# Kernel optimization log

Measured on AMD Instinct MI355X. Metric: run time of the kernel, lower is better.

Reference implementation:

```python
import jax, jax.numpy as jnp
import numpy as np

NUM_LAYERS = 3
CHANNELS = 8
IN_CHANNELS = 8
MASK_OUT_STRIDE = 4


def resize_align_corners(x, oh, ow):
    # Bilinear resize with align_corners=True, x: [N, C, H, W]
    n, c, h, w = x.shape
    ys = jnp.linspace(0.0, h - 1.0, oh)
    xs = jnp.linspace(0.0, w - 1.0, ow)
    y0 = jnp.clip(jnp.floor(ys).astype(jnp.int32), 0, h - 2)
    x0 = jnp.clip(jnp.floor(xs).astype(jnp.int32), 0, w - 2)
    wy = (ys - y0.astype(ys.dtype)).astype(x.dtype)[None, None, :, None]
    wx = (xs - x0.astype(xs.dtype)).astype(x.dtype)[None, None, None, :]
    top = x[:, :, y0, :]
    bot = x[:, :, y0 + 1, :]
    row = top * (1.0 - wy) + bot * wy          # [n,c,oh,w]
    left = row[:, :, :, x0]
    right = row[:, :, :, x0 + 1]
    return left * (1.0 - wx) + right * wx       # [n,c,oh,ow]


def aligned_bilinear(t, factor):
    # Faithful port of adet.utils.comm.aligned_bilinear
    if factor == 1:
        return t
    h, w = t.shape[2], t.shape[3]
    t = jnp.pad(t, ((0, 0), (0, 0), (0, 1), (0, 1)), mode="edge")
    oh, ow = factor * h + 1, factor * w + 1
    t = resize_align_corners(t, oh, ow)
    p = factor // 2
    t = jnp.pad(t, ((0, 0), (0, 0), (p, 0), (p, 0)), mode="edge")
    return t[:, :, : oh - 1, : ow - 1]


def reference(mask_feats, mask_head_params, locations_inst, soi, im_inds, fpn_levels, mask_feat_stride):
    N, C, H, W = mask_feats.shape
    n_inst = mask_head_params.shape[0]
    # compute_locations at mask_feat_stride (x fastest, matching torch meshgrid order)
    half = mask_feat_stride // 2
    sx = jnp.arange(W, dtype=mask_feats.dtype) * mask_feat_stride + half
    sy = jnp.arange(H, dtype=mask_feats.dtype) * mask_feat_stride + half
    gy, gx = jnp.meshgrid(sy, sx, indexing="ij")
    locs = jnp.stack([gx.reshape(-1), gy.reshape(-1)], axis=1)  # [HW, 2]
    # relative coords, normalized by size-of-interest of instance's FPN level
    rel = locations_inst[:, None, :] - locs[None, :, :]          # [n, HW, 2]
    rel = jnp.transpose(rel, (0, 2, 1))                          # [n, 2, HW]
    rel = rel / soi[fpn_levels][:, None, None]
    feats = mask_feats[im_inds].reshape(n_inst, IN_CHANNELS, H * W)
    x = jnp.concatenate([rel.astype(mask_feats.dtype), feats], axis=1)  # [n, 10, HW]
    # parse_dynamic_params: split flat params into per-instance weights/biases
    wn = [(IN_CHANNELS + 2) * CHANNELS, CHANNELS * CHANNELS, CHANNELS * 1]
    bn = [CHANNELS, CHANNELS, 1]
    offs = np.cumsum([0] + wn + bn)
    parts = [mask_head_params[:, offs[i]:offs[i + 1]] for i in range(6)]
    w0 = parts[0].reshape(n_inst, CHANNELS, IN_CHANNELS + 2)
    w1 = parts[1].reshape(n_inst, CHANNELS, CHANNELS)
    w2 = parts[2].reshape(n_inst, 1, CHANNELS)
    b0, b1, b2 = parts[3], parts[4], parts[5]
    # per-instance dynamic MLP (1x1 grouped conv == batched matmul)
    x = jax.nn.relu(jnp.einsum("noi,nip->nop", w0, x) + b0[:, :, None])
    x = jax.nn.relu(jnp.einsum("noi,nip->nop", w1, x) + b1[:, :, None])
    x = jnp.einsum("noi,nip->nop", w2, x) + b2[:, :, None]
    logits = x.reshape(n_inst, 1, H, W)
    factor = int(mask_feat_stride // MASK_OUT_STRIDE)
    return aligned_bilinear(logits, factor)


def setup_inputs() -> dict:
    key = jax.random.key(0)
    k0, k1, k2, k3, k4 = jax.random.split(key, 5)
    N, C, H, W = 4, IN_CHANNELS, 128, 192
    n_inst = 128
    stride = 8
    num_gen_params = (IN_CHANNELS + 2) * CHANNELS + CHANNELS * CHANNELS + CHANNELS + CHANNELS + CHANNELS + 1  # 169
    mask_feats = jax.random.normal(k0, (N, C, H, W), dtype=jnp.float32)
    mask_head_params = jax.random.normal(k1, (n_inst, num_gen_params), dtype=jnp.float32) * 0.1
    locations_inst = jax.random.uniform(k2, (n_inst, 2), dtype=jnp.float32) * jnp.array([W * stride, H * stride], jnp.float32)
    soi = jnp.array([64.0, 128.0, 256.0, 512.0, 1024.0], jnp.float32)
    im_inds = jax.random.randint(k3, (n_inst,), 0, N)
    fpn_levels = jax.random.randint(k4, (n_inst,), 0, 5)
    return {
        "mask_feats": mask_feats,
        "mask_head_params": mask_head_params,
        "locations_inst": locations_inst,
        "soi": soi,
        "im_inds": im_inds,
        "fpn_levels": fpn_levels,
        "mask_feat_stride": stride,
    }
```

## Files before the change

### kernel.cpp

```cpp
#include <hip/hip_runtime.h>

#define HH 128
#define WW 192
#define HW (HH * WW)

typedef float f32x4 __attribute__((ext_vector_type(4)));

__device__ __forceinline__ float relu(float v) { return fmaxf(v, 0.0f); }


__global__ __launch_bounds__(256) void dmh_kernel(
    const float* __restrict__ mask_feats,
    const float* __restrict__ params,
    const float* __restrict__ locs,
    const float* __restrict__ soi,
    const int*   __restrict__ im_inds,
    const int*   __restrict__ fpn_levels,
    const int*   __restrict__ stride_p,
    float*       __restrict__ out)
{
    const int tid = threadIdx.x;
    const int c0 = blockIdx.x * 64;
    const int r0 = blockIdx.y * 32;
    const int n  = blockIdx.z;

    __shared__ float sW[176];
    __shared__ float tile[33 * 66];

    if (tid < 169) {
        float v = params[(size_t)n * 169 + tid];
        int d;
        if (tid < 80)       { int o = tid / 10, r = tid - o * 10;
                              d = (r == 0) ? o : (r == 1) ? (8 + o) : (24 + (r - 2) * 8 + o); }
        else if (tid < 144) { int t = tid - 80, o = t >> 3, i = t & 7; d = 88 + i * 8 + o; }
        else if (tid < 152) d = 152 + (tid - 144);
        else if (tid < 160) d = 16 + (tid - 152);
        else if (tid < 168) d = 160 + (tid - 160);
        else                d = 168;
        sW[d] = v;
    }

    const int   stride = *stride_p;
    const float half   = 0.5f * (float)stride;
    const float locx = locs[2 * n + 0];
    const float locy = locs[2 * n + 1];
    const float inv  = 1.0f / soi[fpn_levels[n]];
    const float* fb  = mask_feats + (size_t)im_inds[n] * 8 * HW;

    const int ir  = (tid >> 4) * 2;
    const int ic  = (tid & 15) * 4;
    const int rA  = r0 + ir;
    const int cc0 = c0 + ic;
    const float* fpA = fb + rA * WW + cc0;

    f32x4 xA[8], xB[8];
    #pragma unroll
    for (int ch = 0; ch < 8; ++ch) {
        xA[ch] = *reinterpret_cast<const f32x4*>(fpA + ch * HW);
        xB[ch] = *reinterpret_cast<const f32x4*>(fpA + ch * HW + WW);
    }

    __syncthreads();

    const f32x4* __restrict__ sW4 = reinterpret_cast<const f32x4*>(sW);

    {
        const float rxd = -(float)stride * inv;
        float rx[4];
        rx[0] = (locx - (float)(cc0 * stride) - half) * inv;
        rx[1] = rx[0] + rxd; rx[2] = rx[1] + rxd; rx[3] = rx[2] + rxd;
        const float ryA = (locy - (float)(rA * stride) - half) * inv;
        const float ryB = ryA - (float)stride * inv;

        f32x4 w0xL = sW4[0], w0xH = sW4[1];
        f32x4 w0yL = sW4[2], w0yH = sW4[3];
        f32x4 b0L  = sW4[4], b0H  = sW4[5];

        float hA[8][4], hB[8][4];
        #pragma unroll
        for (int o = 0; o < 8; ++o) {
            float wx = (o < 4) ? w0xL[o] : w0xH[o - 4];
            float wy = (o < 4) ? w0yL[o] : w0yH[o - 4];
            float b  = (o < 4) ? b0L[o]  : b0H[o - 4];
            float tA = fmaf(wy, ryA, b);
            float tB = fmaf(wy, ryB, b);
            #pragma unroll
            for (int j = 0; j < 4; ++j) {
                hA[o][j] = fmaf(wx, rx[j], tA);
                hB[o][j] = fmaf(wx, rx[j], tB);
            }
        }
        #pragma unroll
        for (int ch = 0; ch < 8; ++ch) {
            f32x4 wL = sW4[6 + 2 * ch];
            f32x4 wH = sW4[7 + 2 * ch];
            #pragma unroll
            for (int o = 0; o < 8; ++o) {
                float w = (o < 4) ? wL[o] : wH[o - 4];
                #pragma unroll
                for (int j = 0; j < 4; ++j) {
                    hA[o][j] = fmaf(w, xA[ch][j], hA[o][j]);
                    hB[o][j] = fmaf(w, xB[ch][j], hB[o][j]);
                }
            }
        }

        float aA[8][4], aB[8][4];
        {
            f32x4 b1L = sW4[40], b1H = sW4[41];
            #pragma unroll
            for (int o = 0; o < 8; ++o) {
                float b = (o < 4) ? b1L[o] : b1H[o - 4];
                #pragma unroll
                for (int j = 0; j < 4; ++j) { aA[o][j] = b; aB[o][j] = b; }
            }
        }
        #pragma unroll
        for (int i = 0; i < 8; ++i) {
            f32x4 wL = sW4[22 + 2 * i];
            f32x4 wH = sW4[23 + 2 * i];
            float vA[4], vB[4];
            #pragma unroll
            for (int j = 0; j < 4; ++j) { vA[j] = relu(hA[i][j]); vB[j] = relu(hB[i][j]); }
            #pragma unroll
            for (int o = 0; o < 8; ++o) {
                float w = (o < 4) ? wL[o] : wH[o - 4];
                #pragma unroll
                for (int j = 0; j < 4; ++j) {
                    aA[o][j] = fmaf(w, vA[j], aA[o][j]);
                    aB[o][j] = fmaf(w, vB[j], aB[o][j]);
                }
            }
        }

        f32x4 w2L = sW4[38], w2H = sW4[39];
        const float b2v = sW[168];
        float lgA[4] = {b2v, b2v, b2v, b2v};
        float lgB[4] = {b2v, b2v, b2v, b2v};
        #pragma unroll
        for (int o = 0; o < 8; ++o) {
            float w2 = (o < 4) ? w2L[o] : w2H[o - 4];
            #pragma unroll
            for (int j = 0; j < 4; ++j) {
                lgA[j] = fmaf(w2, relu(aA[o][j]), lgA[j]);
                lgB[j] = fmaf(w2, relu(aB[o][j]), lgB[j]);
            }
        }
        #pragma unroll
        for (int j = 0; j < 4; ++j) {
            tile[(ir + 1) * 66 + ic + 1 + j] = lgA[j];
            tile[(ir + 2) * 66 + ic + 1 + j] = lgB[j];
        }
    }

    if (tid < 97) {
        int r, c;
        if (tid < 65) { r = -1; c = tid - 1; }
        else          { r = tid - 65; c = -1; }
        int hr = min(max(r0 + r, 0), HH - 1);
        int hc = min(max(c0 + c, 0), WW - 1);
        const float* hfp = fb + hr * WW + hc;
        float rx  = (locx - (float)(hc * stride) - half) * inv;
        float ry2 = (locy - (float)(hr * stride) - half) * inv;
        float hh[8];
        #pragma unroll
        for (int o = 0; o < 8; ++o)
            hh[o] = fmaf(sW[o], rx, fmaf(sW[8 + o], ry2, sW[16 + o]));
        #pragma unroll
        for (int ch = 0; ch < 8; ++ch) {
            float x = hfp[ch * HW];
            #pragma unroll
            for (int o = 0; o < 8; ++o) hh[o] = fmaf(sW[24 + ch * 8 + o], x, hh[o]);
        }
        float aa[8];
        #pragma unroll
        for (int o = 0; o < 8; ++o) aa[o] = sW[160 + o];
        #pragma unroll
        for (int i = 0; i < 8; ++i) {
            float v = relu(hh[i]);
            #pragma unroll
            for (int o = 0; o < 8; ++o) aa[o] = fmaf(sW[88 + i * 8 + o], v, aa[o]);
        }
        float lg = sW[168];
        #pragma unroll
        for (int o = 0; o < 8; ++o) lg = fmaf(sW[152 + o], relu(aa[o]), lg);
        tile[(r + 1) * 66 + (c + 1)] = lg;
    }
    __syncthreads();

    const int kx = tid & 31;
    const int ky = tid >> 5;
    float* ob = out + ((size_t)n * 256 + 2 * r0) * 384 + 2 * c0 + 4 * kx;
    #pragma unroll
    for (int yy = 0; yy < 8; ++yy) {
        int yt = ky * 8 + yy;
        int iy = yt - 1;
        int rbl = iy >> 1;
        int fy = iy & 1;
        float wy0 = fy ? 0.5f : 1.0f;
        float wy1 = fy ? 0.5f : 0.0f;
        int sr  = rbl + 1;
        int sr2 = sr + fy;
        const float* ra = &tile[sr  * 66 + 2 * kx];
        const float* rc = &tile[sr2 * 66 + 2 * kx];
        float t0 = fmaf(wy1, rc[0], wy0 * ra[0]);
        float t1 = fmaf(wy1, rc[1], wy0 * ra[1]);
        float t2 = fmaf(wy1, rc[2], wy0 * ra[2]);
        f32x4 o4;
        o4.x = 0.5f * (t0 + t1);
        o4.y = t1;
        o4.z = 0.5f * (t1 + t2);
        o4.w = t2;
        __builtin_nontemporal_store(o4, reinterpret_cast<f32x4*>(ob + (size_t)yt * 384));
    }
}

extern "C" void kernel_launch(void* const* d_in, const int* in_sizes, int n_in,
                              void* d_out, int out_size, void* d_ws, size_t ws_size,
                              hipStream_t stream) {
    const float* mask_feats = (const float*)d_in[0];
    const float* params     = (const float*)d_in[1];
    const float* locs       = (const float*)d_in[2];
    const float* soi        = (const float*)d_in[3];
    const int*   im_inds    = (const int*)d_in[4];
    const int*   fpn_levels = (const int*)d_in[5];
    const int*   stride_p   = (const int*)d_in[6];
    float* out = (float*)d_out;

    dim3 grid(WW / 64, HH / 32, 128);
    dim3 block(256);
    dmh_kernel<<<grid, block, 0, stream>>>(
        mask_feats, params, locs, soi, im_inds, fpn_levels, stride_p, out);
}
```

Measured before the change: 21.28 us.

## Retile to full-width 16-row strips and drop scalar halo recomputation

Each block now covers a 16-row by full-width (192 column) strip instead of a 32x64 tile, so halo handling needs only one extra row above. That row is clamped, and the left column edge is handled by clamping the index in the upsampling stage. The scalar halo path run by 97 threads is removed; halo rows go through the same vectorized 4-wide per-thread compute as the interior. The first unit's feature loads are hoisted ahead of the weight-scatter barrier to overlap latency. In exchange, the grid has fewer but larger blocks, the redundant halo row costs about 1/16 extra compute, and the last work unit runs only on a partial set of threads.

```diff
diff --git a/kernel.cpp b/kernel.cpp
--- a/kernel.cpp
+++ b/kernel.cpp
@@ -3,6 +3,7 @@
 #define HH 128
 #define WW 192
 #define HW (HH * WW)
+#define TS 196
 
 typedef float f32x4 __attribute__((ext_vector_type(4)));
 
@@ -20,15 +21,33 @@
     float*       __restrict__ out)
 {
     const int tid = threadIdx.x;
-    const int c0 = blockIdx.x * 64;
-    const int r0 = blockIdx.y * 32;
-    const int n  = blockIdx.z;
+    const int r0  = blockIdx.x * 16;
+    const int n   = blockIdx.y;
 
     __shared__ float sW[176];
-    __shared__ float tile[33 * 66];
+    __shared__ float tile[17 * TS];
+
+    float wv = 0.0f;
+    if (tid < 169) wv = params[(size_t)n * 169 + tid];
+
+    const int   stride = *stride_p;
+    const float half_s = 0.5f * (float)stride;
+    const float locx = locs[2 * n + 0];
+    const float locy = locs[2 * n + 1];
+    const float inv  = 1.0f / soi[fpn_levels[n]];
+    const float* fb  = mask_feats + (size_t)im_inds[n] * 8 * HW;
+
+    const int row0 = tid / 48;
+    const int cg0  = tid - row0 * 48;
+    const int srow0 = max(r0 - 1 + row0, 0);
+    const int col00 = cg0 * 4;
+    const float* fp0 = fb + srow0 * WW + col00;
+    f32x4 xv0[8];
+    #pragma unroll
+    for (int ch = 0; ch < 8; ++ch)
+        xv0[ch] = *reinterpret_cast<const f32x4*>(fp0 + ch * HW);
 
     if (tid < 169) {
-        float v = params[(size_t)n * 169 + tid];
         int d;
         if (tid < 80)       { int o = tid / 10, r = tid - o * 10;
                               d = (r == 0) ? o : (r == 1) ? (8 + o) : (24 + (r - 2) * 8 + o); }
@@ -37,58 +56,32 @@
         else if (tid < 160) d = 16 + (tid - 152);
         else if (tid < 168) d = 160 + (tid - 160);
         else                d = 168;
-        sW[d] = v;
+        sW[d] = wv;
     }
-
-    const int   stride = *stride_p;
-    const float half   = 0.5f * (float)stride;
-    const float locx = locs[2 * n + 0];
-    const float locy = locs[2 * n + 1];
-    const float inv  = 1.0f / soi[fpn_levels[n]];
-    const float* fb  = mask_feats + (size_t)im_inds[n] * 8 * HW;
-
-    const int ir  = (tid >> 4) * 2;
-    const int ic  = (tid & 15) * 4;
-    const int rA  = r0 + ir;
-    const int cc0 = c0 + ic;
-    const float* fpA = fb + rA * WW + cc0;
-
-    f32x4 xA[8], xB[8];
-    #pragma unroll
-    for (int ch = 0; ch < 8; ++ch) {
-        xA[ch] = *reinterpret_cast<const f32x4*>(fpA + ch * HW);
-        xB[ch] = *reinterpret_cast<const f32x4*>(fpA + ch * HW + WW);
-    }
-
     __syncthreads();
 
     const f32x4* __restrict__ sW4 = reinterpret_cast<const f32x4*>(sW);
 
-    {
+    auto compute_unit = [&](int row, int col0, int srow, const f32x4* xv) {
         const float rxd = -(float)stride * inv;
         float rx[4];
-        rx[0] = (locx - (float)(cc0 * stride) - half) * inv;
+        rx[0] = (locx - (float)(col0 * stride) - half_s) * inv;
         rx[1] = rx[0] + rxd; rx[2] = rx[1] + rxd; rx[3] = rx[2] + rxd;
-        const float ryA = (locy - (float)(rA * stride) - half) * inv;
-        const float ryB = ryA - (float)stride * inv;
+        const float ry = (locy - (float)(srow * stride) - half_s) * inv;
 
         f32x4 w0xL = sW4[0], w0xH = sW4[1];
         f32x4 w0yL = sW4[2], w0yH = sW4[3];
         f32x4 b0L  = sW4[4], b0H  = sW4[5];
 
-        float hA[8][4], hB[8][4];
+        float h[8][4];
         #pragma unroll
         for (int o = 0; o < 8; ++o) {
             float wx = (o < 4) ? w0xL[o] : w0xH[o - 4];
             float wy = (o < 4) ? w0yL[o] : w0yH[o - 4];
             float b  = (o < 4) ? b0L[o]  : b0H[o - 4];
-            float tA = fmaf(wy, ryA, b);
-            float tB = fmaf(wy, ryB, b);
+            float t  = fmaf(wy, ry, b);
             #pragma unroll
-            for (int j = 0; j < 4; ++j) {
-                hA[o][j] = fmaf(wx, rx[j], tA);
-                hB[o][j] = fmaf(wx, rx[j], tB);
-            }
+            for (int j = 0; j < 4; ++j) h[o][j] = fmaf(wx, rx[j], t);
         }
         #pragma unroll
         for (int ch = 0; ch < 8; ++ch) {
@@ -98,120 +91,92 @@
             for (int o = 0; o < 8; ++o) {
                 float w = (o < 4) ? wL[o] : wH[o - 4];
                 #pragma unroll
-                for (int j = 0; j < 4; ++j) {
-                    hA[o][j] = fmaf(w, xA[ch][j], hA[o][j]);
-                    hB[o][j] = fmaf(w, xB[ch][j], hB[o][j]);
-                }
+                for (int j = 0; j < 4; ++j) h[o][j] = fmaf(w, xv[ch][j], h[o][j]);
             }
         }
-
-        float aA[8][4], aB[8][4];
+        float a[8][4];
         {
             f32x4 b1L = sW4[40], b1H = sW4[41];
             #pragma unroll
             for (int o = 0; o < 8; ++o) {
                 float b = (o < 4) ? b1L[o] : b1H[o - 4];
                 #pragma unroll
-                for (int j = 0; j < 4; ++j) { aA[o][j] = b; aB[o][j] = b; }
+                for (int j = 0; j < 4; ++j) a[o][j] = b;
             }
         }
         #pragma unroll
         for (int i = 0; i < 8; ++i) {
             f32x4 wL = sW4[22 + 2 * i];
             f32x4 wH = sW4[23 + 2 * i];
-            float vA[4], vB[4];
+            float v[4];
             #pragma unroll
-            for (int j = 0; j < 4; ++j) { vA[j] = relu(hA[i][j]); vB[j] = relu(hB[i][j]); }
+            for (int j = 0; j < 4; ++j) v[j] = relu(h[i][j]);
             #pragma unroll
             for (int o = 0; o < 8; ++o) {
                 float w = (o < 4) ? wL[o] : wH[o - 4];
                 #pragma unroll
-                for (int j = 0; j < 4; ++j) {
-                    aA[o][j] = fmaf(w, vA[j], aA[o][j]);
-                    aB[o][j] = fmaf(w, vB[j], aB[o][j]);
-                }
+                for (int j = 0; j < 4; ++j) a[o][j] = fmaf(w, v[j], a[o][j]);
             }
         }
-
         f32x4 w2L = sW4[38], w2H = sW4[39];
         const float b2v = sW[168];
-        float lgA[4] = {b2v, b2v, b2v, b2v};
-        float lgB[4] = {b2v, b2v, b2v, b2v};
+        f32x4 lg = {b2v, b2v, b2v, b2v};
         #pragma unroll
         for (int o = 0; o < 8; ++o) {
             float w2 = (o < 4) ? w2L[o] : w2H[o - 4];
             #pragma unroll
-            for (int j = 0; j < 4; ++j) {
-                lgA[j] = fmaf(w2, relu(aA[o][j]), lgA[j]);
-                lgB[j] = fmaf(w2, relu(aB[o][j]), lgB[j]);
-            }
+            for (int j = 0; j < 4; ++j) lg[j] = fmaf(w2, relu(a[o][j]), lg[j]);
         }
+        *reinterpret_cast<f32x4*>(&tile[row * TS + col0]) = lg;
+    };
+
+    auto do_unit = [&](int u) {
+        int row = u / 48;
+        int cg  = u - row * 48;
+        int srow = max(r0 - 1 + row, 0);
+        int col0 = cg * 4;
+        const float* fp = fb + srow * WW + col0;
+        f32x4 xv[8];
         #pragma unroll
-        for (int j = 0; j < 4; ++j) {
-            tile[(ir + 1) * 66 + ic + 1 + j] = lgA[j];
-            tile[(ir + 2) * 66 + ic + 1 + j] = lgB[j];
-        }
-    }
+        for (int ch = 0; ch < 8; ++ch)
+            xv[ch] = *reinterpret_cast<const f32x4*>(fp + ch * HW);
+        compute_unit(row, col0, srow, xv);
+    };
 
-    if (tid < 97) {
-        int r, c;
-        if (tid < 65) { r = -1; c = tid - 1; }
-        else          { r = tid - 65; c = -1; }
-        int hr = min(max(r0 + r, 0), HH - 1);
-        int hc = min(max(c0 + c, 0), WW - 1);
-        const float* hfp = fb + hr * WW + hc;
-        float rx  = (locx - (float)(hc * stride) - half) * inv;
-        float ry2 = (locy - (float)(hr * stride) - half) * inv;
-        float hh[8];
-        #pragma unroll
-        for (int o = 0; o < 8; ++o)
-            hh[o] = fmaf(sW[o], rx, fmaf(sW[8 + o], ry2, sW[16 + o]));
-        #pragma unroll
-        for (int ch = 0; ch < 8; ++ch) {
-            float x = hfp[ch * HW];
-            #pragma unroll
-            for (int o = 0; o < 8; ++o) hh[o] = fmaf(sW[24 + ch * 8 + o], x, hh[o]);
-        }
-        float aa[8];
-        #pragma unroll
-        for (int o = 0; o < 8; ++o) aa[o] = sW[160 + o];
-        #pragma unroll
-        for (int i = 0; i < 8; ++i) {
-            float v = relu(hh[i]);
-            #pragma unroll
-            for (int o = 0; o < 8; ++o) aa[o] = fmaf(sW[88 + i * 8 + o], v, aa[o]);
-        }
-        float lg = sW[168];
-        #pragma unroll
-        for (int o = 0; o < 8; ++o) lg = fmaf(sW[152 + o], relu(aa[o]), lg);
-        tile[(r + 1) * 66 + (c + 1)] = lg;
-    }
+    compute_unit(row0, col00, srow0, xv0);
+    do_unit(tid + 256);
+    do_unit(tid + 512);
+    if (tid < 48) do_unit(768 + tid);
     __syncthreads();
 
-    const int kx = tid & 31;
-    const int ky = tid >> 5;
-    float* ob = out + ((size_t)n * 256 + 2 * r0) * 384 + 2 * c0 + 4 * kx;
+    const int a8 = tid & 7;
+    const int ro = tid >> 3;
+    const int y  = 2 * r0 + ro;
+    const int iy = y - 1;
+    const int rb = iy >> 1;
+    const int fy = iy & 1;
+    const float wy0 = fy ? 0.5f : 1.0f;
+    const float wy1 = fy ? 0.5f : 0.0f;
+    const int lr  = rb - r0 + 1;
+    const int lr2 = lr + fy;
+    const float* ta = &tile[lr  * TS];
+    const float* tb = &tile[lr2 * TS];
+    float* obr = out + ((size_t)n * 256 + y) * 384;
+
     #pragma unroll
-    for (int yy = 0; yy < 8; ++yy) {
-        int yt = ky * 8 + yy;
-        int iy = yt - 1;
-        int rbl = iy >> 1;
-        int fy = iy & 1;
-        float wy0 = fy ? 0.5f : 1.0f;
-        float wy1 = fy ? 0.5f : 0.0f;
-        int sr  = rbl + 1;
-        int sr2 = sr + fy;
-        const float* ra = &tile[sr  * 66 + 2 * kx];
-        const float* rc = &tile[sr2 * 66 + 2 * kx];
-        float t0 = fmaf(wy1, rc[0], wy0 * ra[0]);
-        float t1 = fmaf(wy1, rc[1], wy0 * ra[1]);
-        float t2 = fmaf(wy1, rc[2], wy0 * ra[2]);
+    for (int q = 0; q < 12; ++q) {
+        int f4 = q * 8 + a8;
+        int m0 = 2 * f4 - 1;
+        int mc = max(m0, 0);
+        float t0 = fmaf(wy1, tb[mc],     wy0 * ta[mc]);
+        float t1 = fmaf(wy1, tb[m0 + 1], wy0 * ta[m0 + 1]);
+        float t2 = fmaf(wy1, tb[m0 + 2], wy0 * ta[m0 + 2]);
         f32x4 o4;
         o4.x = 0.5f * (t0 + t1);
         o4.y = t1;
         o4.z = 0.5f * (t1 + t2);
         o4.w = t2;
-        __builtin_nontemporal_store(o4, reinterpret_cast<f32x4*>(ob + (size_t)yt * 384));
+        __builtin_nontemporal_store(o4, reinterpret_cast<f32x4*>(obr + 4 * f4));
     }
 }
 
@@ -227,7 +192,7 @@
     const int*   stride_p   = (const int*)d_in[6];
     float* out = (float*)d_out;
 
-    dim3 grid(WW / 64, HH / 32, 128);
+    dim3 grid(HH / 16, 128);
     dim3 block(256);
     dmh_kernel<<<grid, block, 0, stream>>>(
         mask_feats, params, locs, soi, im_inds, fpn_levels, stride_p, out);
```

Result: slower. 25.96 us (+22.0%).
